# Optimization experiments

Measured on AMD Instinct MI355X. Metric: run time of the kernel, lower is better.

Reference implementation:

```python
import jax, jax.numpy as jnp
import numpy as np

L, M = 4, 2                      # lmax, mmax
SC, HID = 64, 64                 # sphere_channels, hidden_channels
NH, A, V = 8, 32, 16             # heads, attn_alpha, attn_value channels
OUT = 64                         # output_channels
NM = [L + 1 - m for m in range(M + 1)]   # coeffs per |m|: [5, 4, 3]
MSZ = NM[0] + 2 * sum(NM[1:])            # 19 rotated (mmax-reduced) coeffs
NC = (L + 1) ** 2                        # 25 full spherical coeffs
G = 100                                  # spherical grid points
N_NODES, N_EDGES = 5000, 25000
N_SPECIES, EDGE_DIM = 90, 64
EXTRA = NH * A + HID                     # extra m=0 channels (alpha + s2 gating)
RAD_OUT = sum(NM) * 2 * SC               # radial gating weights per edge


def _ln(x, s, b, eps=1e-6):
    mu = jnp.mean(x, -1, keepdims=True)
    var = jnp.mean((x - mu) ** 2, -1, keepdims=True)
    return (x - mu) * jax.lax.rsqrt(var + eps) * s + b


def _smooth_leaky_relu(x, a=0.2):
    return 0.5 * (1 + a) * x + 0.5 * (1 - a) * x * (2 * jax.nn.sigmoid(x) - 1)


def _so2_conv(x, w0, b0, wm_list, c_in, c_out, rad=None, extra=0):
    # x: [E, MSZ, c_in]; block-diagonal SO(2) convolution over m blocks.
    E = x.shape[0]
    x0 = x[:, :NM[0]].reshape(E, NM[0] * c_in)
    off_rad = 0
    if rad is not None:
        x0 = x0 * rad[:, :NM[0] * c_in]
        off_rad = NM[0] * c_in
    y0 = x0 @ w0 + b0
    outs = [y0[:, :NM[0] * c_out].reshape(E, NM[0], c_out)]
    x_extra = y0[:, NM[0] * c_out:] if extra > 0 else None
    off = NM[0]
    for mi, n in enumerate(NM[1:]):
        xm = x[:, off:off + 2 * n].reshape(E, 2, n * c_in)   # (real, imag)
        if rad is not None:
            xm = xm * rad[:, off_rad:off_rad + n * c_in][:, None, :]
            off_rad += n * c_in
        ym = xm @ wm_list[mi]                                # [E, 2, 2*n*c_out]
        half = n * c_out
        yr, yi = ym[..., :half], ym[..., half:]
        out = jnp.stack([yr[:, 0] - yi[:, 1], yr[:, 1] + yi[:, 0]], 1)
        outs.append(out.reshape(E, 2 * n, c_out))
        off += 2 * n
    return jnp.concatenate(outs, axis=1), x_extra


def _seg_softmax(a, seg, n):
    amax = jax.ops.segment_max(a, seg, num_segments=n)
    amax = jnp.where(jnp.isfinite(amax), amax, 0.0)
    ex = jnp.exp(a - amax[seg])
    den = jax.ops.segment_sum(ex, seg, num_segments=n)
    return ex / (den[seg] + 1e-16)


def _forward(node_feats, edge_distances, wigner, wigner_inv, to_grid_mat,
             from_grid_mat, emb_s, emb_r, rad_w1, rad_b1, rad_ln1_s, rad_ln1_b,
             rad_w2, rad_b2, rad_ln2_s, rad_ln2_b, rad_w3, rad_b3,
             c1_w0, c1_b0, c1_w1, c1_w2, c2_w0, c2_b0, c2_w1, c2_w2,
             an_scale, an_bias, alpha_dot, proj_w, proj_b,
             node_species, senders, receivers):
    n_nodes = node_feats.shape[0]
    # edge scalar embedding: rbf distances + atom embeddings of both endpoints
    edge_embeds = jnp.concatenate(
        (edge_distances, emb_s[node_species[senders]],
         emb_r[node_species[receivers]]), axis=1)           # [E, 192]
    # per-edge spherical features: concat sender/receiver channels
    edge_feats = jnp.concatenate(
        (node_feats[senders], node_feats[receivers]), axis=2)  # [E, NC, 2*SC]
    # rotate into edge-aligned frame (reduces to mmax coefficient set)
    edge_feats = jnp.einsum('emk,ekc->emc', wigner, edge_feats)  # [E, MSZ, 2*SC]
    # radial function -> per-m input gating for SO(2) conv 1
    h = jax.nn.silu(_ln(edge_embeds @ rad_w1 + rad_b1, rad_ln1_s, rad_ln1_b))
    h = jax.nn.silu(_ln(h @ rad_w2 + rad_b2, rad_ln2_s, rad_ln2_b))
    rad = h @ rad_w3 + rad_b3                                # [E, RAD_OUT]
    edge_feats, x0_extra = _so2_conv(edge_feats, c1_w0, c1_b0, (c1_w1, c1_w2),
                                     2 * SC, HID, rad=rad, extra=EXTRA)
    x0_alpha = x0_extra[:, :NH * A]
    x0_gating = x0_extra[:, NH * A:]
    # separable S2 activation: SiLU on sphere grid for l>0, SiLU scalars for l=0
    grid = jax.nn.silu(jnp.einsum('gm,emc->egc', to_grid_mat, edge_feats))
    feats = jnp.einsum('gm,egc->emc', from_grid_mat, grid)
    edge_feats = jnp.concatenate(
        (jax.nn.silu(x0_gating)[:, None, :], feats[:, 1:]), axis=1)
    edge_feats, _ = _so2_conv(edge_feats, c2_w0, c2_b0, (c2_w1, c2_w2),
                              HID, NH * V)                   # [E, MSZ, NH*V]
    # attention weights from extra m=0 channels
    a = x0_alpha.reshape(-1, NH, A)
    a = _smooth_leaky_relu(_ln(a, an_scale, an_bias))
    a = jnp.einsum('bik,ik->bi', a, alpha_dot)
    a = _seg_softmax(a, receivers, n_nodes)                  # [E, NH]
    attn = edge_feats.reshape(-1, MSZ, NH, V) * a[:, None, :, None]
    attn = attn.reshape(-1, MSZ, NH * V)
    # rotate back to global frame and scatter-aggregate onto receivers
    edge_out = jnp.einsum('ekm,emc->ekc', wigner_inv, attn)  # [E, NC, NH*V]
    node_out = jax.ops.segment_sum(edge_out, receivers, num_segments=n_nodes)
    # per-degree linear projection (bias only on l=0 coefficient)
    ls = jnp.concatenate([jnp.full(2 * l + 1, l) for l in range(L + 1)])
    out = jnp.einsum('nmc,mco->nmo', node_out, proj_w[ls])
    return out.at[:, 0, :].add(proj_b)


def setup_inputs():
    ks = iter(jax.random.split(jax.random.key(0), 64))
    def nrm(shape, scale=1.0):
        return jax.random.normal(next(ks), shape, jnp.float32) * scale
    return {
        'node_feats': nrm((N_NODES, NC, SC)),
        'edge_distances': jax.random.uniform(next(ks), (N_EDGES, EDGE_DIM), jnp.float32),
        'wigner': nrm((N_EDGES, MSZ, NC), NC ** -0.5),
        'wigner_inv': nrm((N_EDGES, NC, MSZ), MSZ ** -0.5),
        'to_grid_mat': nrm((G, MSZ), MSZ ** -0.5),
        'from_grid_mat': nrm((G, MSZ), G ** -0.5),
        'emb_s': nrm((N_SPECIES, EDGE_DIM), 0.001),
        'emb_r': nrm((N_SPECIES, EDGE_DIM), 0.001),
        'rad_w1': nrm((3 * EDGE_DIM, 64), (3 * EDGE_DIM) ** -0.5),
        'rad_b1': jnp.zeros((64,), jnp.float32),
        'rad_ln1_s': jnp.ones((64,), jnp.float32),
        'rad_ln1_b': jnp.zeros((64,), jnp.float32),
        'rad_w2': nrm((64, 64), 64 ** -0.5),
        'rad_b2': jnp.zeros((64,), jnp.float32),
        'rad_ln2_s': jnp.ones((64,), jnp.float32),
        'rad_ln2_b': jnp.zeros((64,), jnp.float32),
        'rad_w3': nrm((64, RAD_OUT), 64 ** -0.5),
        'rad_b3': jnp.zeros((RAD_OUT,), jnp.float32),
        'c1_w0': nrm((NM[0] * 2 * SC, NM[0] * HID + EXTRA), (NM[0] * 2 * SC) ** -0.5),
        'c1_b0': jnp.zeros((NM[0] * HID + EXTRA,), jnp.float32),
        'c1_w1': nrm((NM[1] * 2 * SC, 2 * NM[1] * HID), (NM[1] * 2 * SC) ** -0.5),
        'c1_w2': nrm((NM[2] * 2 * SC, 2 * NM[2] * HID), (NM[2] * 2 * SC) ** -0.5),
        'c2_w0': nrm((NM[0] * HID, NM[0] * NH * V), (NM[0] * HID) ** -0.5),
        'c2_b0': jnp.zeros((NM[0] * NH * V,), jnp.float32),
        'c2_w1': nrm((NM[1] * HID, 2 * NM[1] * NH * V), (NM[1] * HID) ** -0.5),
        'c2_w2': nrm((NM[2] * HID, 2 * NM[2] * NH * V), (NM[2] * HID) ** -0.5),
        'an_scale': jnp.ones((A,), jnp.float32),
        'an_bias': jnp.zeros((A,), jnp.float32),
        'alpha_dot': nrm((NH, A), A ** -0.5),
        'proj_w': nrm((L + 1, NH * V, OUT), (NH * V) ** -0.5),
        'proj_b': jnp.zeros((OUT,), jnp.float32),
        'node_species': jax.random.randint(next(ks), (N_NODES,), 0, N_SPECIES),
        'senders': jax.random.randint(next(ks), (N_EDGES,), 0, N_NODES),
        'receivers': jax.random.randint(next(ks), (N_EDGES,), 0, N_NODES),
    }


def reference(node_feats, edge_distances, wigner, wigner_inv, to_grid_mat,
              from_grid_mat, emb_s, emb_r, rad_w1, rad_b1, rad_ln1_s, rad_ln1_b,
              rad_w2, rad_b2, rad_ln2_s, rad_ln2_b, rad_w3, rad_b3,
              c1_w0, c1_b0, c1_w1, c1_w2, c2_w0, c2_b0, c2_w1, c2_w2,
              an_scale, an_bias, alpha_dot, proj_w, proj_b,
              node_species, senders, receivers):
    return _forward(node_feats, edge_distances, wigner, wigner_inv, to_grid_mat,
                    from_grid_mat, emb_s, emb_r, rad_w1, rad_b1, rad_ln1_s,
                    rad_ln1_b, rad_w2, rad_b2, rad_ln2_s, rad_ln2_b, rad_w3,
                    rad_b3, c1_w0, c1_b0, c1_w1, c1_w2, c2_w0, c2_b0, c2_w1,
                    c2_w2, an_scale, an_bias, alpha_dot, proj_w, proj_b,
                    node_species, senders, receivers)
```

## Files before the change

kernel.cpp:

```cpp
#include <hip/hip_runtime.h>
#include <hip/hip_bf16.h>

using bf16 = __hip_bfloat16;

#define EDGES 25000
#define NNODES 5000
#define EPB 4
#define NBLK (EDGES / EPB)

__device__ __forceinline__ float sigmf(float x) { return 1.0f / (1.0f + expf(-x)); }

template<bool BF>
__device__ __forceinline__ float LD1(const void* p, size_t i) {
    if (BF) return __bfloat162float(((const bf16*)p)[i]);
    else    return ((const float*)p)[i];
}

template<bool BF>
__device__ __forceinline__ float4 LD4(const void* p, size_t i) {
    if (BF) {
        ushort4 u = *reinterpret_cast<const ushort4*>((const bf16*)p + i);
        float4 r;
        r.x = __uint_as_float((unsigned)u.x << 16);
        r.y = __uint_as_float((unsigned)u.y << 16);
// ... 95 lines not shown
    if ((*dtf != 0) != BF) return;
    __shared__ __align__(16) float sm[12160];
    float* XE   = sm;
    float* T1   = sm + 768;
    float* H1   = sm + 1024;
    float* T2   = sm + 1280;
    float* H2   = sm + 1536;
    float* rad0 = sm + 1792;
    float* x0   = sm + 4352;
    float* R    = sm + 6912;
    float* extraA = sm + 11136;

    const int t = threadIdx.x;
    const int e0 = blockIdx.x * EPB;
    const int eg = t >> 6, tt = t & 63;

    {
        int ee = e0 + eg;
        XE[eg * 192 + tt]       = LD1<BF>(edge_dist, (size_t)ee * 64 + tt);
        XE[eg * 192 + 64 + tt]  = LD1<BF>(emb_s, (size_t)species[senders[ee]] * 64 + tt);
        XE[eg * 192 + 128 + tt] = LD1<BF>(emb_r, (size_t)species[receivers[ee]] * 64 + tt);
    }
    __syncthreads();
    {
        float a = LD1<BF>(rb1, tt);
        #pragma unroll 4
        for (int k = 0; k < 192; k++) a += XE[eg * 192 + k] * LD1<BF>(rw1, k * 64 + tt);
        T1[eg * 64 + tt] = a;
    }
    __syncthreads();
    {
        float mu = 0.f;
        for (int k = 0; k < 64; k++) mu += T1[eg * 64 + k];
        mu *= (1.f / 64.f);
        float var = 0.f;
        for (int k = 0; k < 64; k++) { float d = T1[eg * 64 + k] - mu; var += d * d; }
        float xn = (T1[eg * 64 + tt] - mu) * rsqrtf(var * (1.f / 64.f) + 1e-6f) * LD1<BF>(rl1s, tt) + LD1<BF>(rl1b, tt);
        H1[eg * 64 + tt] = xn * sigmf(xn);
    }
    __syncthreads();
    {
        float a = LD1<BF>(rb2, tt);
        #pragma unroll 4
        for (int k = 0; k < 64; k++) a += H1[eg * 64 + k] * LD1<BF>(rw2, k * 64 + tt);
        T2[eg * 64 + tt] = a;
    }
    __syncthreads();
    {
        float mu = 0.f;
        for (int k = 0; k < 64; k++) mu += T2[eg * 64 + k];
        mu *= (1.f / 64.f);
        float var = 0.f;
        for (int k = 0; k < 64; k++) { float d = T2[eg * 64 + k] - mu; var += d * d; }
        float xn = (T2[eg * 64 + tt] - mu) * rsqrtf(var * (1.f / 64.f) + 1e-6f) * LD1<BF>(rl2s, tt) + LD1<BF>(rl2b, tt);
        H2[eg * 64 + tt] = xn * sigmf(xn);
    }
    __syncthreads();
    if (t < 160) {
        int j0 = t * 4;
        float4 acc[EPB];
        float4 bv = LD4<BF>(rb3, j0);
        #pragma unroll
        for (int e = 0; e < EPB; e++) acc[e] = bv;
        for (int i = 0; i < 64; i += 4)
            STREAM4_1(rw3, 1536, j0, &H2[e * 64 + i], EPB)
        #pragma unroll
        for (int e = 0; e < EPB; e++) *(float4*)&rad0[e * 640 + j0] = acc[e];
    }
    __syncthreads();
    {
        float* X  = R;
        float* WG = R + 3200;
        for (int e = 0; e < EPB; e++) {
            int s_ = senders[e0 + e], r_ = receivers[e0 + e];
            for (int q = t; q < 800; q += 256) {
                int k = q >> 5, c0 = (q & 31) * 4;
                float4 v = (c0 < 64) ? LD4<BF>(node_feats, (size_t)s_ * 1600 + k * 64 + c0)
                                     : LD4<BF>(node_feats, (size_t)r_ * 1600 + k * 64 + (c0 - 64));
                *(float4*)&X[q * 4] = v;
            }
            for (int i = t; i < 125; i += 256) WG[i] = LD1<BF>(wigner, (size_t)(e0 + e) * 475 + i);
            __syncthreads();
            if (t < 160) {
                int m = t >> 5, c0 = (t & 31) * 4;
                float4 acc = make_float4(0.f, 0.f, 0.f, 0.f);
                #pragma unroll
                for (int k = 0; k < 25; k++) fma4(acc, WG[m * 25 + k], *(const float4*)&X[k * 128 + c0]);
                float4 rv = *(const float4*)&rad0[e * 640 + t * 4];
                acc.x *= rv.x; acc.y *= rv.y; acc.z *= rv.z; acc.w *= rv.w;
                *(float4*)&x0[e * 640 + t * 4] = acc;
            }
            __syncthreads();
        }
    }
    {
        float* Y = R;
        int col = t & 63, kq = t >> 6;
        int j0 = 320 + col * 4;
        int ibase = kq * 160;
        float4 acc[EPB];
        #pragma unroll
        for (int e = 0; e < EPB; e++) acc[e] = make_float4(0.f, 0.f, 0.f, 0.f);
        for (int i = ibase; i < ibase + 160; i += 4)
            STREAM4_1(c1w0, 640, j0, &x0[e * 640 + i], EPB)
        __syncthreads();
        #pragma unroll
        for (int e = 0; e < EPB; e++) *(float4*)&Y[(e * 256 + kq * 64 + col) * 4] = acc[e];
        __syncthreads();
        {
            int e = t >> 6, c = t & 63;
            float4 s = LD4<BF>(c1b0, 320 + c * 4);
            #pragma unroll
            for (int q = 0; q < 4; q++) {
                float4 v = *(const float4*)&Y[(e * 256 + q * 64 + c) * 4];
                s.x += v.x; s.y += v.y; s.z += v.z; s.w += v.w;
            }
            *(float4*)&extraA[e * 256 + c * 4] = s;
        }
    }
    __syncthreads();
    if (t < 32) {
        int e = t >> 3, h = t & 7;
        float mu = 0.0f;
        for (int k = 0; k < 32; k++) mu += extraA[e * 256 + h * 32 + k];
        mu *= (1.0f / 32.0f);
        float var = 0.0f;
        for (int k = 0; k < 32; k++) { float d = extraA[e * 256 + h * 32 + k] - mu; var += d * d; }
        float rs = rsqrtf(var * (1.0f / 32.0f) + 1e-6f);
        float logit = 0.0f;
        for (int k = 0; k < 32; k++) {
            float xn = (extraA[e * 256 + h * 32 + k] - mu) * rs * LD1<BF>(an_s, k) + LD1<BF>(an_b, k);
            float slr = 0.6f * xn + 0.4f * xn * (2.0f * sigmf(xn) - 1.0f);
            logit += slr * LD1<BF>(adot, h * 32 + k);
        }
        int r = receivers[e0 + e];
        alpha_out[(size_t)(e0 + e) * 8 + h] = logit;
        atomicMax(&nmax[r * 8 + h], encF(logit));
    }
}

__global__ void k_exp(const int* __restrict__ receivers, const unsigned* __restrict__ nmax,
                      float* __restrict__ alpha, float* __restrict__ nden) {
    int tid = blockIdx.x * 256 + threadIdx.x;
    if (tid >= EDGES * 8) return;
    int e = tid >> 3, h = tid & 7;
    int r = receivers[e];
    float m = decF(nmax[r * 8 + h]);
    float ex = expf(alpha[tid] - m);
    alpha[tid] = ex;
    atomicAdd(&nden[r * 8 + h], ex);
}

template<bool BF>
__global__ __launch_bounds__(256, 2) void k_mega2(
    const void* __restrict__ node_feats, const void* __restrict__ edge_dist,
    const void* __restrict__ wigner, const void* __restrict__ wigner_inv,
    const void* __restrict__ to_grid, const void* __restrict__ from_grid,
    const void* __restrict__ emb_s, const void* __restrict__ emb_r,
    const void* __restrict__ rw1, const void* __restrict__ rb1,
    const void* __restrict__ rl1s, const void* __restrict__ rl1b,
    const void* __restrict__ rw2, const void* __restrict__ rb2,
    const void* __restrict__ rl2s, const void* __restrict__ rl2b,
    const void* __restrict__ rw3, const void* __restrict__ rb3,
    const void* __restrict__ c1w0, const void* __restrict__ c1b0,
    const void* __restrict__ c1w1, const void* __restrict__ c1w2,
    const void* __restrict__ c2w0, const void* __restrict__ c2b0,
    const void* __restrict__ c2w1, const void* __restrict__ c2w2,
    const void* __restrict__ proj_w,
    const int* __restrict__ species, const int* __restrict__ senders,
    const int* __restrict__ receivers, const int* __restrict__ dtf,
    const float* __restrict__ alpha, const float* __restrict__ nden,
    float* __restrict__ accb)
{
    if ((*dtf != 0) != BF) return;
    __shared__ __align__(16) float sm[19744];
    float* Q   = sm;
    float* C   = sm + 9728;
    float* RAD = sm + 13408;
    float* YF  = sm + 14592;
    float* GAT = sm + 19456;
    float* ALs = sm + 19712;

    const int t = threadIdx.x;
    const int e0 = blockIdx.x * EPB;
    int snd[EPB], rcv[EPB];
    #pragma unroll
    for (int e = 0; e < EPB; e++) { snd[e] = senders[e0 + e]; rcv[e] = receivers[e0 + e]; }

    {
        float* XE = C;
        float* T1 = C + 768;
        float* H1 = C + 1024;
        float* T2 = C + 1280;
        float* H2 = C + 1536;
        const int eg = t >> 6, tt = t & 63;
        {
            int ee = e0 + eg;
            XE[eg * 192 + tt]       = LD1<BF>(edge_dist, (size_t)ee * 64 + tt);
            XE[eg * 192 + 64 + tt]  = LD1<BF>(emb_s, (size_t)species[senders[ee]] * 64 + tt);
            XE[eg * 192 + 128 + tt] = LD1<BF>(emb_r, (size_t)species[receivers[ee]] * 64 + tt);
        }
        __syncthreads();
        {
            float a = LD1<BF>(rb1, tt);
            #pragma unroll 4
            for (int k = 0; k < 192; k++) a += XE[eg * 192 + k] * LD1<BF>(rw1, k * 64 + tt);
            T1[eg * 64 + tt] = a;
        }
        __syncthreads();
        {
            float mu = 0.f;
            for (int k = 0; k < 64; k++) mu += T1[eg * 64 + k];
            mu *= (1.f / 64.f);
            float var = 0.f;
            for (int k = 0; k < 64; k++) { float d = T1[eg * 64 + k] - mu; var += d * d; }
            float xn = (T1[eg * 64 + tt] - mu) * rsqrtf(var * (1.f / 64.f) + 1e-6f) * LD1<BF>(rl1s, tt) + LD1<BF>(rl1b, tt);
            H1[eg * 64 + tt] = xn * sigmf(xn);
        }
        __syncthreads();
        {
            float a = LD1<BF>(rb2, tt);
            #pragma unroll 4
            for (int k = 0; k < 64; k++) a += H1[eg * 64 + k] * LD1<BF>(rw2, k * 64 + tt);
            T2[eg * 64 + tt] = a;
        }
        __syncthreads();
        {
            float mu = 0.f;
            for (int k = 0; k < 64; k++) mu += T2[eg * 64 + k];
            mu *= (1.f / 64.f);
            float var = 0.f;
            for (int k = 0; k < 64; k++) { float d = T2[eg * 64 + k] - mu; var += d * d; }
            float xn = (T2[eg * 64 + tt] - mu) * rsqrtf(var * (1.f / 64.f) + 1e-6f) * LD1<BF>(rl2s, tt) + LD1<BF>(rl2b, tt);
            H2[eg * 64 + tt] = xn * sigmf(xn);
        }
        __syncthreads();
        for (int qq = t; qq < 384; qq += 256) {
            int j0 = qq * 4;
            float4 acc[EPB];
            float4 bv = LD4<BF>(rb3, j0);
            #pragma unroll
            for (int e = 0; e < EPB; e++) acc[e] = bv;
            for (int i = 0; i < 64; i += 4)
                STREAM4_1(rw3, 1536, j0, &H2[e * 64 + i], EPB)
            #pragma unroll
            for (int e = 0; e < EPB; e++) *(float4*)&RAD[e * 1536 + j0] = acc[e];
        }
        __syncthreads();
    }

    {
        float* X  = C;
        float* WG = C + 3200;
        for (int e = 0; e < EPB; e++) {
            int s_ = senders[e0 + e], r_ = receivers[e0 + e];
            for (int q = t; q < 800; q += 256) {
                int k = q >> 5, c0 = (q & 31) * 4;
                float4 v = (c0 < 64) ? LD4<BF>(node_feats, (size_t)s_ * 1600 + k * 64 + c0)
                                     : LD4<BF>(node_feats, (size_t)r_ * 1600 + k * 64 + (c0 - 64));
                *(float4*)&X[q * 4] = v;
            }
            for (int i = t; i < 475; i += 256) WG[i] = LD1<BF>(wigner, (size_t)(e0 + e) * 475 + i);
            __syncthreads();
            for (int q = t; q < 608; q += 256) {
                int m = q >> 5, c0 = (q & 31) * 4;
                float4 acc = make_float4(0.f, 0.f, 0.f, 0.f);
                #pragma unroll
                for (int k = 0; k < 25; k++) fma4(acc, WG[m * 25 + k], *(const float4*)&X[k * 128 + c0]);
                int ri0;
                if (m < 5)       ri0 = m * 128 + c0;
                else if (m < 13) ri0 = 640 + ((m - 5) & 3) * 128 + c0;
                else             ri0 = 1152 + ((m - 13) % 3) * 128 + c0;
                float4 rv = *(const float4*)&RAD[e * 1536 + ri0];
                acc.x *= rv.x; acc.y *= rv.y; acc.z *= rv.z; acc.w *= rv.w;
                *(float4*)&Q[e * 2432 + q * 4] = acc;
            }
            __syncthreads();
        }
    }

    float4 ra[EPB], rb[EPB];
    {
        float* EF2 = C;
        float* YM  = YF;
        {
            int r = t >> 7, cg = t & 127;
            int j0 = cg * 4;
            int abase = 640 + 512 * r;
            float4 acc[EPB];
            #pragma unroll
            for (int e = 0; e < EPB; e++) acc[e] = make_float4(0.f, 0.f, 0.f, 0.f);
            for (int i = 0; i < 512; i += 4)
                STREAM4_1(c1w1, 512, j0, &Q[e * 2432 + abase + i], EPB)
            #pragma unroll
            for (int e = 0; e < EPB; e++) *(float4*)&YM[e * 1024 + r * 512 + j0] = acc[e];
        }
        __syncthreads();
        for (int u = t; u < 1024; u += 256) {
            int e = u >> 8, j = u & 255;
            float y0l = YM[e * 1024 + j];
            float y0u = YM[e * 1024 + 256 + j];
            float y1l = YM[e * 1024 + 512 + j];
            float y1u = YM[e * 1024 + 768 + j];
            EF2[e * 1216 + 320 + j] = y0l - y1u;
            EF2[e * 1216 + 576 + j] = y1l + y0u;
        }
        __syncthreads();
        if (t < 96) {
            int jq = (t < 80) ? t : (144 + (t - 80));
            int j0 = jq * 4;
            float4 acc[EPB];
            float4 bv = LD4<BF>(c1b0, j0);
            #pragma unroll
            for (int e = 0; e < EPB; e++) acc[e] = bv;
            for (int i = 0; i < 640; i += 4)
                STREAM4_1(c1w0, 640, j0, &Q[e * 2432 + i], EPB)
            if (t < 80) {
                #pragma unroll
                for (int e = 0; e < EPB; e++) *(float4*)&EF2[e * 1216 + j0] = acc[e];
            } else {
                #pragma unroll
                for (int e = 0; e < EPB; e++) *(float4*)&GAT[e * 64 + (t - 80) * 4] = acc[e];
            }
        } else if (t < 192) {
            int j0 = (t - 96) * 4;
            #pragma unroll
            for (int e = 0; e < EPB; e++) { ra[e] = make_float4(0,0,0,0); rb[e] = make_float4(0,0,0,0); }
            for (int i = 0; i < 384; i += 4)
                STREAM4_2(c1w2, 384, j0, &Q[e * 2432 + 1664 + i], &Q[e * 2432 + 2048 + i])
            if (j0 >= 192) {
                #pragma unroll
                for (int e = 0; e < EPB; e++) {
                    *(float4*)&YF[e * 192 + (j0 - 192)] = ra[e];
                    *(float4*)&YF[768 + e * 192 + (j0 - 192)] = rb[e];
                }
            }
        }
        __syncthreads();
        if (t >= 96 && t < 144) {
            int j0 = (t - 96) * 4;
            #pragma unroll
            for (int e = 0; e < EPB; e++) {
                float4 y0u = *(const float4*)&YF[e * 192 + j0];
                float4 y1u = *(const float4*)&YF[768 + e * 192 + j0];
                float4 r, im;
                r.x = ra[e].x - y1u.x; r.y = ra[e].y - y1u.y; r.z = ra[e].z - y1u.z; r.w = ra[e].w - y1u.w;
                im.x = rb[e].x + y0u.x; im.y = rb[e].y + y0u.y; im.z = rb[e].z + y0u.z; im.w = rb[e].w + y0u.w;
                *(float4*)&EF2[e * 1216 + 832 + j0] = r;
                *(float4*)&EF2[e * 1216 + 1024 + j0] = im;
            }
        }
        __syncthreads();
    }

    {
        float* FE  = YF;
        float* G   = Q;
        float* S2  = Q + 6400;
        float* EF2 = C;
        for (int e = 0; e < EPB; e++) {
            for (int idx = t; idx < 1600; idx += 256) {
                int gi = idx >> 4, c0 = (idx & 15) * 4;
                float4 acc = make_float4(0.f, 0.f, 0.f, 0.f);
                #pragma unroll
                for (int m = 0; m < 19; m++)
                    fma4(acc, LD1<BF>(to_grid, gi * 19 + m),
                         *(const float4*)&EF2[e * 1216 + m * 64 + c0]);
                silu4(acc);
                *(float4*)&G[gi * 64 + c0] = acc;
            }
            __syncthreads();
            for (int idx = t; idx < 608; idx += 256) {
                int m = idx >> 5, cq = (idx >> 1) & 15, h = idx & 1, c0 = cq * 4;
                int g0 = h * 50;
                float4 acc = make_float4(0.f, 0.f, 0.f, 0.f);
                #pragma unroll 5
                for (int gi = 0; gi < 50; gi++)
                    fma4(acc, LD1<BF>(from_grid, (g0 + gi) * 19 + m),
                         *(const float4*)&G[(g0 + gi) * 64 + c0]);
                *(float4*)&S2[idx * 4] = acc;
            }
            __syncthreads();
            for (int idx = t; idx < 304; idx += 256) {
                int m = idx >> 4, cq = idx & 15;
                int pb = (m * 32 + cq * 2) * 4;
                float4 a = *(const float4*)&S2[pb];
                float4 b = *(const float4*)&S2[pb + 4];
                a.x += b.x; a.y += b.y; a.z += b.z; a.w += b.w;
                *(float4*)&FE[e * 1216 + m * 64 + cq * 4] = a;
            }
            __syncthreads();
        }
        if (t < 64) {
            #pragma unroll
            for (int e = 0; e < EPB; e++) { float x = GAT[e * 64 + t]; FE[e * 1216 + t] = x * sigmf(x); }
        }
        __syncthreads();
    }

    {
        float* FE = YF;
        if (t < 160) {
            int j0 = t * 4;
            float4 acc[EPB];
            float4 bv = LD4<BF>(c2b0, j0);
            #pragma unroll
            for (int e = 0; e < EPB; e++) acc[e] = bv;
            for (int i = 0; i < 320; i += 4)
                STREAM4_1(c2w0, 640, j0, &FE[e * 1216 + i], EPB)
            #pragma unroll
            for (int e = 0; e < EPB; e++) *(float4*)&Q[e * 2432 + j0] = acc[e];
        }
        {
            int j0 = t * 4;
            #pragma unroll
            for (int e = 0; e < EPB; e++) { ra[e] = make_float4(0,0,0,0); rb[e] = make_float4(0,0,0,0); }
            for (int i = 0; i < 256; i += 4)
                STREAM4_2(c2w1, 1024, j0, &FE[e * 1216 + 320 + i], &FE[e * 1216 + 576 + i])
            if (j0 >= 512) {
                #pragma unroll
                for (int e = 0; e < EPB; e++) {
                    *(float4*)&C[e * 512 + (j0 - 512)] = ra[e];
                    *(float4*)&C[2048 + e * 512 + (j0 - 512)] = rb[e];
                }
            }
        }
        __syncthreads();
        if (t < 128) {
            int j0 = t * 4;
            #pragma unroll
            for (int e = 0; e < EPB; e++) {
                float4 y0u = *(const float4*)&C[e * 512 + j0];
                float4 y1u = *(const float4*)&C[2048 + e * 512 + j0];
                float4 r, im;
                r.x = ra[e].x - y1u.x; r.y = ra[e].y - y1u.y; r.z = ra[e].z - y1u.z; r.w = ra[e].w - y1u.w;
                im.x = rb[e].x + y0u.x; im.y = rb[e].y + y0u.y; im.z = rb[e].z + y0u.z; im.w = rb[e].w + y0u.w;
                *(float4*)&Q[e * 2432 + 640 + j0] = r;
                *(float4*)&Q[e * 2432 + 1152 + j0] = im;
            }
        }
        __syncthreads();
        if (t < 192) {
            int j0 = t * 4;
            #pragma unroll
            for (int e = 0; e < EPB; e++) { ra[e] = make_float4(0,0,0,0); rb[e] = make_float4(0,0,0,0); }
            for (int i = 0; i < 192; i += 4)
                STREAM4_2(c2w2, 768, j0, &FE[e * 1216 + 832 + i], &FE[e * 1216 + 1024 + i])
            if (j0 >= 384) {
                #pragma unroll
                for (int e = 0; e < EPB; e++) {
                    *(float4*)&C[e * 384 + (j0 - 384)] = ra[e];
                    *(float4*)&C[1536 + e * 384 + (j0 - 384)] = rb[e];
                }
            }
        }
        __syncthreads();
        if (t < 96) {
            int j0 = t * 4;
            #pragma unroll
            for (int e = 0; e < EPB; e++) {
                float4 y0u = *(const float4*)&C[e * 384 + j0];
                float4 y1u = *(const float4*)&C[1536 + e * 384 + j0];
                float4 r, im;
                r.x = ra[e].x - y1u.x; r.y = ra[e].y - y1u.y; r.z = ra[e].z - y1u.z; r.w = ra[e].w - y1u.w;
                im.x = rb[e].x + y0u.x; im.y = rb[e].y + y0u.y; im.z = rb[e].z + y0u.z; im.w = rb[e].w + y0u.w;
                *(float4*)&Q[e * 2432 + 1664 + j0] = r;
                *(float4*)&Q[e * 2432 + 2048 + j0] = im;
            }
        }
        __syncthreads();
    }

    {
        float* WV = C;
        float* EO = C + 1920;
        if (t < 32) {
            int h = t & 7;
            int ee = e0 + (t >> 3);
            ALs[t] = alpha[(size_t)ee * 8 + h] / (nden[(size_t)receivers[ee] * 8 + h] + 1e-16f);
        }
        for (int i = t; i < 1900; i += 256) {
            int e = i / 475, j = i - e * 475;
            WV[e * 480 + j] = LD1<BF>(wigner_inv, (size_t)(e0 + e) * 475 + j);
        }
        __syncthreads();
        for (int kb = 0; kb < 25; kb += 13) {
            const int nk = (kb == 0) ? 13 : 12;
            for (int u = t; u < nk * 128; u += 256) {
                int e = u & 3, idx = u >> 2;
                int ki = idx >> 5, c0 = (idx & 31) * 4;
                int k = kb + ki;
                float4 acc = make_float4(0.f, 0.f, 0.f, 0.f);
                #pragma unroll
                for (int m = 0; m < 19; m++)
                    fma4(acc, WV[e * 480 + k * 19 + m], *(const float4*)&Q[e * 2432 + m * 128 + c0]);
                float al = ALs[e * 8 + (c0 >> 4)];
                int b = (ki * 128 + c0) * 4 + e;
                EO[b + 0]  = acc.x * al;
                EO[b + 4]  = acc.y * al;
                EO[b + 8]  = acc.z * al;
                EO[b + 12] = acc.w * al;
            }
            __syncthreads();
            if (t < nk * 16) {
                int ki = t >> 4, o0 = (t & 15) * 4;
                int k = kb + ki;
                int l = (k == 0) ? 0 : (k < 4) ? 1 : (k < 9) ? 2 : (k < 16) ? 3 : 4;
                float4 pa0 = make_float4(0,0,0,0), pa1 = pa0, pa2 = pa0, pa3 = pa0;
                const float* eob = &EO[ki * 512];
                size_t base = (size_t)l * 8192 + o0;
                for (int c = 0; c < 128; c += 4) {
                    float4 p0 = LD4<BF>(proj_w, base + (size_t)(c + 0) * 64);
                    float4 p1 = LD4<BF>(proj_w, base + (size_t)(c + 1) * 64);
                    float4 p2 = LD4<BF>(proj_w, base + (size_t)(c + 2) * 64);
                    float4 p3 = LD4<BF>(proj_w, base + (size_t)(c + 3) * 64);
                    float4 v0 = *(const float4*)&eob[(c + 0) * 4];
                    float4 v1 = *(const float4*)&eob[(c + 1) * 4];
                    float4 v2 = *(const float4*)&eob[(c + 2) * 4];
                    float4 v3 = *(const float4*)&eob[(c + 3) * 4];
                    fma4(pa0, v0.x, p0); fma4(pa1, v0.y, p0); fma4(pa2, v0.z, p0); fma4(pa3, v0.w, p0);
                    fma4(pa0, v1.x, p1); fma4(pa1, v1.y, p1); fma4(pa2, v1.z, p1); fma4(pa3, v1.w, p1);
                    fma4(pa0, v2.x, p2); fma4(pa1, v2.y, p2); fma4(pa2, v2.z, p2); fma4(pa3, v2.w, p2);
                    fma4(pa0, v3.x, p3); fma4(pa1, v3.y, p3); fma4(pa2, v3.z, p3); fma4(pa3, v3.w, p3);
                }
                float* d0 = &accb[(size_t)rcv[0] * 1600 + k * 64 + o0];
                atomicAdd(d0 + 0, pa0.x); atomicAdd(d0 + 1, pa0.y);
                atomicAdd(d0 + 2, pa0.z); atomicAdd(d0 + 3, pa0.w);
                float* d1 = &accb[(size_t)rcv[1] * 1600 + k * 64 + o0];
                atomicAdd(d1 + 0, pa1.x); atomicAdd(d1 + 1, pa1.y);
                atomicAdd(d1 + 2, pa1.z); atomicAdd(d1 + 3, pa1.w);
                float* d2 = &accb[(size_t)rcv[2] * 1600 + k * 64 + o0];
                atomicAdd(d2 + 0, pa2.x); atomicAdd(d2 + 1, pa2.y);
                atomicAdd(d2 + 2, pa2.z); atomicAdd(d2 + 3, pa2.w);
                float* d3 = &accb[(size_t)rcv[3] * 1600 + k * 64 + o0];
                atomicAdd(d3 + 0, pa3.x); atomicAdd(d3 + 1, pa3.y);
                atomicAdd(d3 + 2, pa3.z); atomicAdd(d3 + 3, pa3.w);
            }
            __syncthreads();
        }
    }
}

template<bool BF>
__global__ void k_out(const float* __restrict__ accb, const void* __restrict__ proj_b,
                      void* __restrict__ out, const int* __restrict__ dtf) {
    if ((*dtf != 0) != BF) return;
    int i = blockIdx.x * 256 + threadIdx.x;
    if (i >= NNODES * 1600) return;
    int r = i % 1600;
    int m = r >> 6, o = r & 63;
    float v = accb[i] + ((m == 0) ? LD1<BF>(proj_b, o) : 0.0f);
    if (BF) ((bf16*)out)[i] = __float2bfloat16(v);
    else    ((float*)out)[i] = v;
}

extern "C" void kernel_launch(void* const* d_in, const int* in_sizes, int n_in,
                              void* d_out, int out_size, void* d_ws, size_t ws_size,
                              hipStream_t stream) {
    const void* node_feats = d_in[0];
    const void* edge_dist  = d_in[1];
    const void* wigner     = d_in[2];
    const void* wigner_inv = d_in[3];
    const void* to_grid    = d_in[4];
    const void* from_grid  = d_in[5];
    const void* emb_s      = d_in[6];
    const void* emb_r      = d_in[7];
    const void* rw1  = d_in[8];
    const void* rb1  = d_in[9];
    const void* rl1s = d_in[10];
    const void* rl1b = d_in[11];
    const void* rw2  = d_in[12];
    const void* rb2  = d_in[13];
    const void* rl2s = d_in[14];
    const void* rl2b = d_in[15];
    const void* rw3  = d_in[16];
    const void* rb3  = d_in[17];
    const void* c1w0 = d_in[18];
    const void* c1b0 = d_in[19];
    const void* c1w1 = d_in[20];
    const void* c1w2 = d_in[21];
    const void* c2w0 = d_in[22];
    const void* c2b0 = d_in[23];
    const void* c2w1 = d_in[24];
    const void* c2w2 = d_in[25];
    const void* an_s = d_in[26];
    const void* an_b = d_in[27];
    const void* adot = d_in[28];
    const void* proj_w = d_in[29];
    const void* proj_b = d_in[30];
    const int* species   = (const int*)d_in[31];
    const int* senders   = (const int*)d_in[32];
    const int* receivers = (const int*)d_in[33];

    char* ws = (char*)d_ws;
    float*    accb  = (float*)ws;
    float*    alpha = (float*)(ws + 32000000);
    unsigned* nmax  = (unsigned*)(ws + 32800000);
    float*    nden  = (float*)(ws + 32960000);
    int*      dtf   = (int*)(ws + 33120000);

    k_detect<<<1, 64, 0, stream>>>(edge_dist, dtf);
    k_fill<<<(NNODES * 1600 + 255) / 256, 256, 0, stream>>>(accb, nden, nmax);

    k_alpha<true><<<NBLK, 256, 0, stream>>>(
        node_feats, edge_dist, wigner, emb_s, emb_r,
        rw1, rb1, rl1s, rl1b, rw2, rb2, rl2s, rl2b, rw3, rb3,
        c1w0, c1b0, an_s, an_b, adot, species, senders, receivers, dtf,
        alpha, nmax);
    k_alpha<false><<<NBLK, 256, 0, stream>>>(
        node_feats, edge_dist, wigner, emb_s, emb_r,
        rw1, rb1, rl1s, rl1b, rw2, rb2, rl2s, rl2b, rw3, rb3,
        c1w0, c1b0, an_s, an_b, adot, species, senders, receivers, dtf,
        alpha, nmax);

    k_exp<<<(EDGES * 8 + 255) / 256, 256, 0, stream>>>(receivers, nmax, alpha, nden);

    k_mega2<true><<<NBLK, 256, 0, stream>>>(
        node_feats, edge_dist, wigner, wigner_inv, to_grid, from_grid, emb_s, emb_r,
        rw1, rb1, rl1s, rl1b, rw2, rb2, rl2s, rl2b, rw3, rb3,
        c1w0, c1b0, c1w1, c1w2, c2w0, c2b0, c2w1, c2w2, proj_w,
        species, senders, receivers, dtf, alpha, nden, accb);
    k_mega2<false><<<NBLK, 256, 0, stream>>>(
        node_feats, edge_dist, wigner, wigner_inv, to_grid, from_grid, emb_s, emb_r,
        rw1, rb1, rl1s, rl1b, rw2, rb2, rl2s, rl2b, rw3, rb3,
        c1w0, c1b0, c1w1, c1w2, c2w0, c2b0, c2w1, c2w2, proj_w,
        species, senders, receivers, dtf, alpha, nden, accb);

    k_out<true><<<(NNODES * 1600 + 255) / 256, 256, 0, stream>>>(accb, proj_b, d_out, dtf);
    k_out<false><<<(NNODES * 1600 + 255) / 256, 256, 0, stream>>>(accb, proj_b, d_out, dtf);
}
```

Measured before the change: 4.748 ms.

## Double k_mega2 block to 512 threads and split GEMM reductions across thread halves

Raises k_mega2's block size from 256 to 512 threads and reassigns work to the extra threads. The SO(2) convolution GEMMs split their K dimension or their real/imaginary outputs across thread groups and combine partials through shared memory. The final projection now gives each thread two edges instead of four. The aim is more parallelism per edge block and shorter serial streaming loops over the weights. The cost is extra __syncthreads and partial-sum traffic, idle threads in the small phases, and possible register pressure from the (512,4) launch bounds, which is also a shared-memory occupancy question given the ~79KB static allocation.

```diff
diff --git a/kernel.cpp b/kernel.cpp
--- a/kernel.cpp
+++ b/kernel.cpp
@@ -271,7 +271,7 @@
 }
 
 template<bool BF>
-__global__ __launch_bounds__(256, 2) void k_mega2(
+__global__ __launch_bounds__(512, 4) void k_mega2(
     const void* __restrict__ node_feats, const void* __restrict__ edge_dist,
     const void* __restrict__ wigner, const void* __restrict__ wigner_inv,
     const void* __restrict__ to_grid, const void* __restrict__ from_grid,
@@ -302,9 +302,9 @@
 
     const int t = threadIdx.x;
     const int e0 = blockIdx.x * EPB;
-    int snd[EPB], rcv[EPB];
+    int rcv[EPB];
     #pragma unroll
-    for (int e = 0; e < EPB; e++) { snd[e] = senders[e0 + e]; rcv[e] = receivers[e0 + e]; }
+    for (int e = 0; e < EPB; e++) rcv[e] = receivers[e0 + e];
 
     {
         float* XE = C;
@@ -312,22 +312,25 @@
         float* H1 = C + 1024;
         float* T2 = C + 1280;
         float* H2 = C + 1536;
+        for (int i = t; i < 768; i += 512) {
+            int e = i / 192, j = i - e * 192;
+            int ee = e0 + e;
+            float v;
+            if (j < 64)       v = LD1<BF>(edge_dist, (size_t)ee * 64 + j);
+            else if (j < 128) v = LD1<BF>(emb_s, (size_t)species[senders[ee]] * 64 + (j - 64));
+            else              v = LD1<BF>(emb_r, (size_t)species[receivers[ee]] * 64 + (j - 128));
+            XE[e * 192 + j] = v;
+        }
+        __syncthreads();
         const int eg = t >> 6, tt = t & 63;
-        {
-            int ee = e0 + eg;
-            XE[eg * 192 + tt]       = LD1<BF>(edge_dist, (size_t)ee * 64 + tt);
-            XE[eg * 192 + 64 + tt]  = LD1<BF>(emb_s, (size_t)species[senders[ee]] * 64 + tt);
-            XE[eg * 192 + 128 + tt] = LD1<BF>(emb_r, (size_t)species[receivers[ee]] * 64 + tt);
-        }
-        __syncthreads();
-        {
+        if (t < 256) {
             float a = LD1<BF>(rb1, tt);
             #pragma unroll 4
             for (int k = 0; k < 192; k++) a += XE[eg * 192 + k] * LD1<BF>(rw1, k * 64 + tt);
             T1[eg * 64 + tt] = a;
         }
         __syncthreads();
-        {
+        if (t < 256) {
             float mu = 0.f;
             for (int k = 0; k < 64; k++) mu += T1[eg * 64 + k];
             mu *= (1.f / 64.f);
@@ -337,14 +340,14 @@
             H1[eg * 64 + tt] = xn * sigmf(xn);
         }
         __syncthreads();
-        {
+        if (t < 256) {
             float a = LD1<BF>(rb2, tt);
             #pragma unroll 4
             for (int k = 0; k < 64; k++) a += H1[eg * 64 + k] * LD1<BF>(rw2, k * 64 + tt);
             T2[eg * 64 + tt] = a;
         }
         __syncthreads();
-        {
+        if (t < 256) {
             float mu = 0.f;
             for (int k = 0; k < 64; k++) mu += T2[eg * 64 + k];
             mu *= (1.f / 64.f);
@@ -354,8 +357,8 @@
             H2[eg * 64 + tt] = xn * sigmf(xn);
         }
         __syncthreads();
-        for (int qq = t; qq < 384; qq += 256) {
-            int j0 = qq * 4;
+        if (t < 384) {
+            int j0 = t * 4;
             float4 acc[EPB];
             float4 bv = LD4<BF>(rb3, j0);
             #pragma unroll
@@ -373,15 +376,15 @@
         float* WG = C + 3200;
         for (int e = 0; e < EPB; e++) {
             int s_ = senders[e0 + e], r_ = receivers[e0 + e];
-            for (int q = t; q < 800; q += 256) {
+            for (int q = t; q < 800; q += 512) {
                 int k = q >> 5, c0 = (q & 31) * 4;
                 float4 v = (c0 < 64) ? LD4<BF>(node_feats, (size_t)s_ * 1600 + k * 64 + c0)
                                      : LD4<BF>(node_feats, (size_t)r_ * 1600 + k * 64 + (c0 - 64));
                 *(float4*)&X[q * 4] = v;
             }
-            for (int i = t; i < 475; i += 256) WG[i] = LD1<BF>(wigner, (size_t)(e0 + e) * 475 + i);
-            __syncthreads();
-            for (int q = t; q < 608; q += 256) {
+            if (t < 475) WG[t] = LD1<BF>(wigner, (size_t)(e0 + e) * 475 + t);
+            __syncthreads();
+            for (int q = t; q < 608; q += 512) {
                 int m = q >> 5, c0 = (q & 31) * 4;
                 float4 acc = make_float4(0.f, 0.f, 0.f, 0.f);
                 #pragma unroll
@@ -399,77 +402,123 @@
     }
 
     float4 ra[EPB], rb[EPB];
+
     {
         float* EF2 = C;
         float* YM  = YF;
         {
-            int r = t >> 7, cg = t & 127;
+            int cg = t & 127, r = (t >> 7) & 1, kh = t >> 8;
             int j0 = cg * 4;
-            int abase = 640 + 512 * r;
             float4 acc[EPB];
             #pragma unroll
             for (int e = 0; e < EPB; e++) acc[e] = make_float4(0.f, 0.f, 0.f, 0.f);
-            for (int i = 0; i < 512; i += 4)
-                STREAM4_1(c1w1, 512, j0, &Q[e * 2432 + abase + i], EPB)
+            int kb0 = 256 * kh;
+            for (int i = kb0; i < kb0 + 256; i += 4)
+                STREAM4_1(c1w1, 512, j0, &Q[e * 2432 + 640 + 512 * r + i], EPB)
+            if (kh == 1) {
+                #pragma unroll
+                for (int e = 0; e < EPB; e++) *(float4*)&YM[(e * 2 + r) * 512 + j0] = acc[e];
+            }
+            __syncthreads();
+            if (kh == 0) {
+                #pragma unroll
+                for (int e = 0; e < EPB; e++) {
+                    float4 p = *(const float4*)&YM[(e * 2 + r) * 512 + j0];
+                    acc[e].x += p.x; acc[e].y += p.y; acc[e].z += p.z; acc[e].w += p.w;
+                    *(float4*)&YM[(e * 2 + r) * 512 + j0] = acc[e];
+                }
+            }
+            __syncthreads();
+            for (int u = t; u < 1024; u += 512) {
+                int e = u >> 8, j = u & 255;
+                float y0l = YM[(e * 2 + 0) * 512 + j];
+                float y0u = YM[(e * 2 + 0) * 512 + 256 + j];
+                float y1l = YM[(e * 2 + 1) * 512 + j];
+                float y1u = YM[(e * 2 + 1) * 512 + 256 + j];
+                EF2[e * 1216 + 320 + j] = y0l - y1u;
+                EF2[e * 1216 + 576 + j] = y1l + y0u;
+            }
+            __syncthreads();
+        }
+        {
+            float* MS  = YF;
+            float* M2S = YF + 1536;
+            float4 keep[EPB];
             #pragma unroll
-            for (int e = 0; e < EPB; e++) *(float4*)&YM[e * 1024 + r * 512 + j0] = acc[e];
-        }
-        __syncthreads();
-        for (int u = t; u < 1024; u += 256) {
-            int e = u >> 8, j = u & 255;
-            float y0l = YM[e * 1024 + j];
-            float y0u = YM[e * 1024 + 256 + j];
-            float y1l = YM[e * 1024 + 512 + j];
-            float y1u = YM[e * 1024 + 768 + j];
-            EF2[e * 1216 + 320 + j] = y0l - y1u;
-            EF2[e * 1216 + 576 + j] = y1l + y0u;
-        }
-        __syncthreads();
-        if (t < 96) {
-            int jq = (t < 80) ? t : (144 + (t - 80));
-            int j0 = jq * 4;
-            float4 acc[EPB];
-            float4 bv = LD4<BF>(c1b0, j0);
-            #pragma unroll
-            for (int e = 0; e < EPB; e++) acc[e] = bv;
-            for (int i = 0; i < 640; i += 4)
-                STREAM4_1(c1w0, 640, j0, &Q[e * 2432 + i], EPB)
-            if (t < 80) {
-                #pragma unroll
-                for (int e = 0; e < EPB; e++) *(float4*)&EF2[e * 1216 + j0] = acc[e];
-            } else {
-                #pragma unroll
-                for (int e = 0; e < EPB; e++) *(float4*)&GAT[e * 64 + (t - 80) * 4] = acc[e];
-            }
-        } else if (t < 192) {
-            int j0 = (t - 96) * 4;
-            #pragma unroll
-            for (int e = 0; e < EPB; e++) { ra[e] = make_float4(0,0,0,0); rb[e] = make_float4(0,0,0,0); }
-            for (int i = 0; i < 384; i += 4)
-                STREAM4_2(c1w2, 384, j0, &Q[e * 2432 + 1664 + i], &Q[e * 2432 + 2048 + i])
-            if (j0 >= 192) {
+            for (int e = 0; e < EPB; e++) keep[e] = make_float4(0.f, 0.f, 0.f, 0.f);
+            if (t < 192) {
+                int kh = (t >= 96) ? 1 : 0;
+                int jq = t - 96 * kh;
+                int cmj = (jq < 80) ? jq * 4 : 576 + (jq - 80) * 4;
+                float4 acc[EPB];
+                #pragma unroll
+                for (int e = 0; e < EPB; e++) acc[e] = make_float4(0.f, 0.f, 0.f, 0.f);
+                int kb0 = kh * 320;
+                for (int i = kb0; i < kb0 + 320; i += 4)
+                    STREAM4_1(c1w0, 640, cmj, &Q[e * 2432 + i], EPB)
+                if (kh) {
+                    #pragma unroll
+                    for (int e = 0; e < EPB; e++) *(float4*)&MS[(e * 96 + jq) * 4] = acc[e];
+                } else {
+                    #pragma unroll
+                    for (int e = 0; e < EPB; e++) keep[e] = acc[e];
+                }
+            } else if (t < 384) {
+                int u = t - 192;
+                int r = (u >= 96) ? 1 : 0, cg = u - 96 * r;
+                int j0 = cg * 4;
+                float4 acc[EPB];
+                #pragma unroll
+                for (int e = 0; e < EPB; e++) acc[e] = make_float4(0.f, 0.f, 0.f, 0.f);
+                int abase = 1664 + 384 * r;
+                for (int i = 0; i < 384; i += 4)
+                    STREAM4_1(c1w2, 384, j0, &Q[e * 2432 + abase + i], EPB)
+                if (cg >= 48) {
+                    #pragma unroll
+                    for (int e = 0; e < EPB; e++)
+                        *(float4*)&M2S[((e * 2 + r) * 48 + (cg - 48)) * 4] = acc[e];
+                } else {
+                    #pragma unroll
+                    for (int e = 0; e < EPB; e++) keep[e] = acc[e];
+                }
+            }
+            __syncthreads();
+            if (t < 96) {
+                int jq = t;
+                int cmj = (jq < 80) ? jq * 4 : 576 + (jq - 80) * 4;
+                float4 bv = LD4<BF>(c1b0, cmj);
                 #pragma unroll
                 for (int e = 0; e < EPB; e++) {
-                    *(float4*)&YF[e * 192 + (j0 - 192)] = ra[e];
-                    *(float4*)&YF[768 + e * 192 + (j0 - 192)] = rb[e];
+                    float4 p = *(const float4*)&MS[(e * 96 + jq) * 4];
+                    float4 v;
+                    v.x = keep[e].x + p.x + bv.x; v.y = keep[e].y + p.y + bv.y;
+                    v.z = keep[e].z + p.z + bv.z; v.w = keep[e].w + p.w + bv.w;
+                    if (jq < 80) *(float4*)&EF2[e * 1216 + jq * 4] = v;
+                    else         *(float4*)&GAT[e * 64 + (jq - 80) * 4] = v;
                 }
-            }
-        }
-        __syncthreads();
-        if (t >= 96 && t < 144) {
-            int j0 = (t - 96) * 4;
-            #pragma unroll
-            for (int e = 0; e < EPB; e++) {
-                float4 y0u = *(const float4*)&YF[e * 192 + j0];
-                float4 y1u = *(const float4*)&YF[768 + e * 192 + j0];
-                float4 r, im;
-                r.x = ra[e].x - y1u.x; r.y = ra[e].y - y1u.y; r.z = ra[e].z - y1u.z; r.w = ra[e].w - y1u.w;
-                im.x = rb[e].x + y0u.x; im.y = rb[e].y + y0u.y; im.z = rb[e].z + y0u.z; im.w = rb[e].w + y0u.w;
-                *(float4*)&EF2[e * 1216 + 832 + j0] = r;
-                *(float4*)&EF2[e * 1216 + 1024 + j0] = im;
-            }
-        }
-        __syncthreads();
+            } else if (t >= 192 && t < 384) {
+                int u = t - 192;
+                int r = (u >= 96) ? 1 : 0, cg = u - 96 * r;
+                if (cg < 48) {
+                    int j0 = cg * 4;
+                    #pragma unroll
+                    for (int e = 0; e < EPB; e++) {
+                        float4 o = *(const float4*)&M2S[((e * 2 + (1 - r)) * 48 + cg) * 4];
+                        float4 v;
+                        if (r == 0) {
+                            v.x = keep[e].x - o.x; v.y = keep[e].y - o.y;
+                            v.z = keep[e].z - o.z; v.w = keep[e].w - o.w;
+                            *(float4*)&EF2[e * 1216 + 832 + j0] = v;
+                        } else {
+                            v.x = keep[e].x + o.x; v.y = keep[e].y + o.y;
+                            v.z = keep[e].z + o.z; v.w = keep[e].w + o.w;
+                            *(float4*)&EF2[e * 1216 + 1024 + j0] = v;
+                        }
+                    }
+                }
+            }
+            __syncthreads();
+        }
     }
 
     {
@@ -478,7 +527,7 @@
         float* S2  = Q + 6400;
         float* EF2 = C;
         for (int e = 0; e < EPB; e++) {
-            for (int idx = t; idx < 1600; idx += 256) {
+            for (int idx = t; idx < 1600; idx += 512) {
                 int gi = idx >> 4, c0 = (idx & 15) * 4;
                 float4 acc = make_float4(0.f, 0.f, 0.f, 0.f);
                 #pragma unroll
@@ -489,7 +538,7 @@
                 *(float4*)&G[gi * 64 + c0] = acc;
             }
             __syncthreads();
-            for (int idx = t; idx < 608; idx += 256) {
+            for (int idx = t; idx < 608; idx += 512) {
                 int m = idx >> 5, cq = (idx >> 1) & 15, h = idx & 1, c0 = cq * 4;
                 int g0 = h * 50;
                 float4 acc = make_float4(0.f, 0.f, 0.f, 0.f);
@@ -500,8 +549,8 @@
                 *(float4*)&S2[idx * 4] = acc;
             }
             __syncthreads();
-            for (int idx = t; idx < 304; idx += 256) {
-                int m = idx >> 4, cq = idx & 15;
+            if (t < 304) {
+                int m = t >> 4, cq = t & 15;
                 int pb = (m * 32 + cq * 2) * 4;
                 float4 a = *(const float4*)&S2[pb];
                 float4 b = *(const float4*)&S2[pb + 4];
@@ -518,76 +567,91 @@
     }
 
     {
-        float* FE = YF;
-        if (t < 160) {
-            int j0 = t * 4;
+        float* FE  = YF;
+        float* M1S = C;
+        float4 keep[EPB];
+        {
+            int cg = t & 255, r = t >> 8;
+            int j0 = cg * 4;
             float4 acc[EPB];
-            float4 bv = LD4<BF>(c2b0, j0);
             #pragma unroll
-            for (int e = 0; e < EPB; e++) acc[e] = bv;
-            for (int i = 0; i < 320; i += 4)
-                STREAM4_1(c2w0, 640, j0, &FE[e * 1216 + i], EPB)
-            #pragma unroll
-            for (int e = 0; e < EPB; e++) *(float4*)&Q[e * 2432 + j0] = acc[e];
+            for (int e = 0; e < EPB; e++) acc[e] = make_float4(0.f, 0.f, 0.f, 0.f);
+            int abase = 320 + 256 * r;
+            for (int i = 0; i < 256; i += 4)
+                STREAM4_1(c2w1, 1024, j0, &FE[e * 1216 + abase + i], EPB)
+            if (cg >= 128) {
+                #pragma unroll
+                for (int e = 0; e < EPB; e++)
+                    *(float4*)&M1S[((e * 2 + r) * 128 + (cg - 128)) * 4] = acc[e];
+            } else {
+                #pragma unroll
+                for (int e = 0; e < EPB; e++) keep[e] = acc[e];
+            }
+            __syncthreads();
+            if (cg < 128) {
+                #pragma unroll
+                for (int e = 0; e < EPB; e++) {
+                    float4 o = *(const float4*)&M1S[((e * 2 + (1 - r)) * 128 + cg) * 4];
+                    float4 v;
+                    if (r == 0) {
+                        v.x = keep[e].x - o.x; v.y = keep[e].y - o.y;
+                        v.z = keep[e].z - o.z; v.w = keep[e].w - o.w;
+                        *(float4*)&Q[e * 2432 + 640 + j0] = v;
+                    } else {
+                        v.x = keep[e].x + o.x; v.y = keep[e].y + o.y;
+                        v.z = keep[e].z + o.z; v.w = keep[e].w + o.w;
+                        *(float4*)&Q[e * 2432 + 1152 + j0] = v;
+                    }
+                }
+            }
+            __syncthreads();
         }
         {
-            int j0 = t * 4;
-            #pragma unroll
-            for (int e = 0; e < EPB; e++) { ra[e] = make_float4(0,0,0,0); rb[e] = make_float4(0,0,0,0); }
-            for (int i = 0; i < 256; i += 4)
-                STREAM4_2(c2w1, 1024, j0, &FE[e * 1216 + 320 + i], &FE[e * 1216 + 576 + i])
-            if (j0 >= 512) {
+            float* M2S = C;
+            if (t < 160) {
+                int j0 = t * 4;
+                float4 acc[EPB];
+                float4 bv = LD4<BF>(c2b0, j0);
+                #pragma unroll
+                for (int e = 0; e < EPB; e++) acc[e] = bv;
+                for (int i = 0; i < 320; i += 4)
+                    STREAM4_1(c2w0, 640, j0, &FE[e * 1216 + i], EPB)
+                #pragma unroll
+                for (int e = 0; e < EPB; e++) *(float4*)&Q[e * 2432 + j0] = acc[e];
+            } else if (t < 352) {
+                int cg = t - 160;
+                int j0 = cg * 4;
+                #pragma unroll
+                for (int e = 0; e < EPB; e++) { ra[e] = make_float4(0,0,0,0); rb[e] = make_float4(0,0,0,0); }
+                for (int i = 0; i < 192; i += 4)
+                    STREAM4_2(c2w2, 768, j0, &FE[e * 1216 + 832 + i], &FE[e * 1216 + 1024 + i])
+                if (cg >= 96) {
+                    #pragma unroll
+                    for (int e = 0; e < EPB; e++) {
+                        *(float4*)&M2S[((e * 2 + 0) * 96 + (cg - 96)) * 4] = ra[e];
+                        *(float4*)&M2S[((e * 2 + 1) * 96 + (cg - 96)) * 4] = rb[e];
+                    }
+                }
+            }
+            __syncthreads();
+            if (t >= 160 && t < 256) {
+                int cg = t - 160;
+                int j0 = cg * 4;
                 #pragma unroll
                 for (int e = 0; e < EPB; e++) {
-                    *(float4*)&C[e * 512 + (j0 - 512)] = ra[e];
-                    *(float4*)&C[2048 + e * 512 + (j0 - 512)] = rb[e];
+                    float4 y1u = *(const float4*)&M2S[((e * 2 + 1) * 96 + cg) * 4];
+                    float4 y0u = *(const float4*)&M2S[((e * 2 + 0) * 96 + cg) * 4];
+                    float4 r, im;
+                    r.x = ra[e].x - y1u.x; r.y = ra[e].y - y1u.y;
+                    r.z = ra[e].z - y1u.z; r.w = ra[e].w - y1u.w;
+                    im.x = rb[e].x + y0u.x; im.y = rb[e].y + y0u.y;
+                    im.z = rb[e].z + y0u.z; im.w = rb[e].w + y0u.w;
+                    *(float4*)&Q[e * 2432 + 1664 + j0] = r;
+                    *(float4*)&Q[e * 2432 + 2048 + j0] = im;
                 }
             }
-        }
-        __syncthreads();
-        if (t < 128) {
-            int j0 = t * 4;
-            #pragma unroll
-            for (int e = 0; e < EPB; e++) {
-                float4 y0u = *(const float4*)&C[e * 512 + j0];
-                float4 y1u = *(const float4*)&C[2048 + e * 512 + j0];
-                float4 r, im;
-                r.x = ra[e].x - y1u.x; r.y = ra[e].y - y1u.y; r.z = ra[e].z - y1u.z; r.w = ra[e].w - y1u.w;
-                im.x = rb[e].x + y0u.x; im.y = rb[e].y + y0u.y; im.z = rb[e].z + y0u.z; im.w = rb[e].w + y0u.w;
-                *(float4*)&Q[e * 2432 + 640 + j0] = r;
-                *(float4*)&Q[e * 2432 + 1152 + j0] = im;
-            }
-        }
-        __syncthreads();
-        if (t < 192) {
-            int j0 = t * 4;
-            #pragma unroll
-            for (int e = 0; e < EPB; e++) { ra[e] = make_float4(0,0,0,0); rb[e] = make_float4(0,0,0,0); }
-            for (int i = 0; i < 192; i += 4)
-                STREAM4_2(c2w2, 768, j0, &FE[e * 1216 + 832 + i], &FE[e * 1216 + 1024 + i])
-            if (j0 >= 384) {
-                #pragma unroll
-                for (int e = 0; e < EPB; e++) {
-                    *(float4*)&C[e * 384 + (j0 - 384)] = ra[e];
-                    *(float4*)&C[1536 + e * 384 + (j0 - 384)] = rb[e];
-                }
-            }
-        }
-        __syncthreads();
-        if (t < 96) {
-            int j0 = t * 4;
-            #pragma unroll
-            for (int e = 0; e < EPB; e++) {
-                float4 y0u = *(const float4*)&C[e * 384 + j0];
-                float4 y1u = *(const float4*)&C[1536 + e * 384 + j0];
-                float4 r, im;
-                r.x = ra[e].x - y1u.x; r.y = ra[e].y - y1u.y; r.z = ra[e].z - y1u.z; r.w = ra[e].w - y1u.w;
-                im.x = rb[e].x + y0u.x; im.y = rb[e].y + y0u.y; im.z = rb[e].z + y0u.z; im.w = rb[e].w + y0u.w;
-                *(float4*)&Q[e * 2432 + 1664 + j0] = r;
-                *(float4*)&Q[e * 2432 + 2048 + j0] = im;
-            }
-        }
-        __syncthreads();
+            __syncthreads();
+        }
     }
 
     {
@@ -598,14 +662,14 @@
             int ee = e0 + (t >> 3);
             ALs[t] = alpha[(size_t)ee * 8 + h] / (nden[(size_t)receivers[ee] * 8 + h] + 1e-16f);
         }
-        for (int i = t; i < 1900; i += 256) {
+        for (int i = t; i < 1900; i += 512) {
             int e = i / 475, j = i - e * 475;
             WV[e * 480 + j] = LD1<BF>(wigner_inv, (size_t)(e0 + e) * 475 + j);
         }
         __syncthreads();
         for (int kb = 0; kb < 25; kb += 13) {
             const int nk = (kb == 0) ? 13 : 12;
-            for (int u = t; u < nk * 128; u += 256) {
+            for (int u = t; u < nk * 128; u += 512) {
                 int e = u & 3, idx = u >> 2;
                 int ki = idx >> 5, c0 = (idx & 31) * 4;
                 int k = kb + ki;
@@ -621,39 +685,33 @@
                 EO[b + 12] = acc.w * al;
             }
             __syncthreads();
-            if (t < nk * 16) {
-                int ki = t >> 4, o0 = (t & 15) * 4;
+            if (t < nk * 32) {
+                int ki = t >> 5;
+                int rem = t & 31;
+                int o = rem >> 1, eh = rem & 1;
+                int o0 = o * 4;
                 int k = kb + ki;
                 int l = (k == 0) ? 0 : (k < 4) ? 1 : (k < 9) ? 2 : (k < 16) ? 3 : 4;
-                float4 pa0 = make_float4(0,0,0,0), pa1 = pa0, pa2 = pa0, pa3 = pa0;
-                const float* eob = &EO[ki * 512];
+                float4 pa0 = make_float4(0,0,0,0), pa1 = pa0;
+                const float* eob = &EO[ki * 512 + eh * 2];
                 size_t base = (size_t)l * 8192 + o0;
                 for (int c = 0; c < 128; c += 4) {
                     float4 p0 = LD4<BF>(proj_w, base + (size_t)(c + 0) * 64);
                     float4 p1 = LD4<BF>(proj_w, base + (size_t)(c + 1) * 64);
                     float4 p2 = LD4<BF>(proj_w, base + (size_t)(c + 2) * 64);
                     float4 p3 = LD4<BF>(proj_w, base + (size_t)(c + 3) * 64);
-                    float4 v0 = *(const float4*)&eob[(c + 0) * 4];
-                    float4 v1 = *(const float4*)&eob[(c + 1) * 4];
-                    float4 v2 = *(const float4*)&eob[(c + 2) * 4];
-                    float4 v3 = *(const float4*)&eob[(c + 3) * 4];
-                    fma4(pa0, v0.x, p0); fma4(pa1, v0.y, p0); fma4(pa2, v0.z, p0); fma4(pa3, v0.w, p0);
-                    fma4(pa0, v1.x, p1); fma4(pa1, v1.y, p1); fma4(pa2, v1.z, p1); fma4(pa3, v1.w, p1);
-                    fma4(pa0, v2.x, p2); fma4(pa1, v2.y, p2); fma4(pa2, v2.z, p2); fma4(pa3, v2.w, p2);
-                    fma4(pa0, v3.x, p3); fma4(pa1, v3.y, p3); fma4(pa2, v3.z, p3); fma4(pa3, v3.w, p3);
+                    fma4(pa0, eob[(c + 0) * 4], p0); fma4(pa1, eob[(c + 0) * 4 + 1], p0);
+                    fma4(pa0, eob[(c + 1) * 4], p1); fma4(pa1, eob[(c + 1) * 4 + 1], p1);
+                    fma4(pa0, eob[(c + 2) * 4], p2); fma4(pa1, eob[(c + 2) * 4 + 1], p2);
+                    fma4(pa0, eob[(c + 3) * 4], p3); fma4(pa1, eob[(c + 3) * 4 + 1], p3);
                 }
-                float* d0 = &accb[(size_t)rcv[0] * 1600 + k * 64 + o0];
+                int ep = eh * 2;
+                float* d0 = &accb[(size_t)rcv[ep] * 1600 + k * 64 + o0];
                 atomicAdd(d0 + 0, pa0.x); atomicAdd(d0 + 1, pa0.y);
                 atomicAdd(d0 + 2, pa0.z); atomicAdd(d0 + 3, pa0.w);
-                float* d1 = &accb[(size_t)rcv[1] * 1600 + k * 64 + o0];
+                float* d1 = &accb[(size_t)rcv[ep + 1] * 1600 + k * 64 + o0];
                 atomicAdd(d1 + 0, pa1.x); atomicAdd(d1 + 1, pa1.y);
                 atomicAdd(d1 + 2, pa1.z); atomicAdd(d1 + 3, pa1.w);
-                float* d2 = &accb[(size_t)rcv[2] * 1600 + k * 64 + o0];
-                atomicAdd(d2 + 0, pa2.x); atomicAdd(d2 + 1, pa2.y);
-                atomicAdd(d2 + 2, pa2.z); atomicAdd(d2 + 3, pa2.w);
-                float* d3 = &accb[(size_t)rcv[3] * 1600 + k * 64 + o0];
-                atomicAdd(d3 + 0, pa3.x); atomicAdd(d3 + 1, pa3.y);
-                atomicAdd(d3 + 2, pa3.z); atomicAdd(d3 + 3, pa3.w);
             }
             __syncthreads();
         }
@@ -734,12 +792,12 @@
 
     k_exp<<<(EDGES * 8 + 255) / 256, 256, 0, stream>>>(receivers, nmax, alpha, nden);
 
-    k_mega2<true><<<NBLK, 256, 0, stream>>>(
+    k_mega2<true><<<NBLK, 512, 0, stream>>>(
         node_feats, edge_dist, wigner, wigner_inv, to_grid, from_grid, emb_s, emb_r,
         rw1, rb1, rl1s, rl1b, rw2, rb2, rl2s, rl2b, rw3, rb3,
         c1w0, c1b0, c1w1, c1w2, c2w0, c2b0, c2w1, c2w2, proj_w,
         species, senders, receivers, dtf, alpha, nden, accb);
-    k_mega2<false><<<NBLK, 256, 0, stream>>>(
+    k_mega2<false><<<NBLK, 512, 0, stream>>>(
         node_feats, edge_dist, wigner, wigner_inv, to_grid, from_grid, emb_s, emb_r,
         rw1, rb1, rl1s, rl1b, rw2, rb2, rl2s, rl2b, rw3, rb3,
         c1w0, c1b0, c1w1, c1w2, c2w0, c2b0, c2w1, c2w2, proj_w,
```

After: 4.283 ms. 9.8% less time.
